# Kernel tuning notes

Hardware: AMD Instinct MI355X
Metric: run time of the kernel (lower is better)

## Reference

```python
import jax, jax.numpy as jnp
import numpy as np

TOP_K = 512  # int(node_num * K) = int(2048 * 0.25)
NEG = -1.0e12
SLOPE = 0.01  # nn.LeakyReLU default negative_slope


def setup_inputs() -> dict:
    key = jax.random.key(0)
    k1, k2, k3, k4 = jax.random.split(key, 4)
    B, N, in_c, out_c, gs = 8, 2048, 128, 128, 128
    x = jax.random.normal(k1, (B, N, in_c), dtype=jnp.float32)
    W = jax.random.normal(k2, (in_c, out_c), dtype=jnp.float32) * (1.0 / np.sqrt(in_c))
    a = jax.random.normal(k3, (2 * out_c, 1), dtype=jnp.float32) * (1.0 / np.sqrt(2 * out_c))
    GL = jax.random.normal(k4, (N, gs), dtype=jnp.float32) * (1.0 / np.sqrt(gs))
    return {"x": x, "W": W, "a": a, "GL": GL}


def reference(x, W, a, GL):
    B, N, _ = x.shape
    out_c = W.shape[1]
    # learned adjacency: softmax(relu(GL GL^T)) + I  -> [N, N]
    adj = jax.nn.softmax(jax.nn.relu(GL @ GL.T), axis=-1) + jnp.eye(N, dtype=GL.dtype)
    h = x @ W  # [B, N, out_c]
    # e[b,i,j] = LeakyReLU( [h_i ; h_j] . a ) = LeakyReLU( h_i.a1 + h_j.a2 )
    # (avoids materializing the [B, N*N, 2*out_c] concat of the original)
    a1, a2 = a[:out_c, 0], a[out_c:, 0]
    e = jax.nn.leaky_relu((h @ a1)[:, :, None] + (h @ a2)[:, None, :], SLOPE)  # [B,N,N]
    att = jnp.where(adj[None] > 0, e, NEG)
    # top-k along dim=1 (rows, per column j): transpose so that axis is last
    att_t = jnp.swapaxes(att, 1, 2)  # [B, Nj, Ni]
    _, idx = jax.lax.top_k(att_t, TOP_K)  # idx: [B, Nj, TOP_K]
    b_ix = jnp.arange(B)[:, None, None]
    j_ix = jnp.arange(N)[None, :, None]
    mask_t = jnp.zeros_like(att_t).at[b_ix, j_ix, idx].set(1.0)
    mask = jnp.swapaxes(mask_t, 1, 2)  # [B, Ni, Nj]
    att = jax.nn.softmax(att * mask, axis=2)
    h_prime = jax.nn.relu(att @ h)  # [B, N, out_c]
    return jnp.swapaxes(h_prime, -2, -1)  # [B, out_c, N]
```

## Files before the change

### kernel.cpp

```cpp
#include <hip/hip_runtime.h>
#include <hip/hip_bf16.h>
#include <math.h>


#define B_ 8
#define N_ 2048
#define C_ 128
#define TOPK_ 512
#define NCH_ 32
#define CL_ 64
#define NP1_ 2050

#define H_OFF    ((size_t)0)
#define P_OFF    (H_OFF + (size_t)B_*N_*C_)
#define Q_OFF    (P_OFF + (size_t)B_*N_)
#define QS_OFF   (Q_OFF + (size_t)B_*N_)
#define US_OFF   (QS_OFF + (size_t)B_*N_)
#define VS_OFF   (US_OFF + (size_t)B_*N_)
#define SRT_OFF  (VS_OFF + (size_t)B_*N_)
#define SUS_OFF  (SRT_OFF + (size_t)B_*N_)
#define PVS_OFF  (SUS_OFF + (size_t)B_*NP1_)
#define SUL_OFF  (PVS_OFF + (size_t)B_*NP1_)
#define PVL_OFF  (SUL_OFF + (size_t)B_*N_*128)
#define TOTU_OFF (PVL_OFF + (size_t)B_*N_*128)
#define TOTV_OFF (TOTU_OFF + (size_t)B_*NCH_*128)
#define MR_OFF   (TOTV_OFF + (size_t)B_*NCH_*128)
#define MPART_OFF (MR_OFF + (size_t)B_*C_)
#define PTHR_OFF (MPART_OFF + (size_t)B_*32*C_)
#define ITHR_OFF (PTHR_OFF + (size_t)B_)

__device__ __forceinline__ unsigned enc_f(float f) {
  unsigned b = __float_as_uint(f);
  return b ^ ((b >> 31) ? 0xFFFFFFFFu : 0x80000000u);
}
__device__ __forceinline__ float dec_f(unsigned e) {
  unsigned b = (e & 0x80000000u) ? (e ^ 0x80000000u) : ~e;
  return __uint_as_float(b);
}
__device__ __forceinline__ unsigned long long sxor64(unsigned long long v, int m) {
  int lo = __shfl_xor((int)(unsigned)(v & 0xffffffffULL), m, 64);
  int hi = __shfl_xor((int)(unsigned)(v >> 32), m, 64);
  return (((unsigned long long)(unsigned)hi) << 32) | (unsigned)lo;
}

__global__ __launch_bounds__(256) void k_gemm(const float* __restrict__ x,
                                              const float* __restrict__ W,
                                              const float* __restrict__ a,
                                              float* __restrict__ h,
                                              float* __restrict__ p,
                                              float* __restrict__ q,
                                              float* __restrict__ mpart) {
  __shared__ float Wl[64 * 128];
  __shared__ float xl[64 * 68];
  __shared__ float a1l[128], a2l[128];
  __shared__ float redp[64][16], redq[64][16];
  const int t = threadIdx.x;
  const int r0 = blockIdx.x * 64;
  if (t < 128) { a1l[t] = a[t]; a2l[t] = a[128 + t]; }
  const int cg = t & 15, rp = t >> 4;
  float acc[4][8];
#pragma unroll
  for (int r = 0; r < 4; ++r)
#pragma unroll
    for (int j = 0; j < 8; ++j) acc[r][j] = 0.f;

  for (int kc = 0; kc < 2; ++kc) {
    __syncthreads();
    const float4* W4 = (const float4*)(W + (size_t)kc * 64 * 128);
    float4* Wl4 = (float4*)Wl;
#pragma unroll
    for (int i = 0; i < 8; ++i) Wl4[t + 256 * i] = W4[t + 256 * i];
#pragma unroll
    for (int i = 0; i < 4; ++i) {
      int idx = t + 256 * i;
      int row = idx >> 4, c4i = idx & 15;
      float4 v = *(const float4*)(x + (size_t)(r0 + row) * 128 + kc * 64 + c4i * 4);
      ((float4*)xl)[row * 17 + c4i] = v;
    }
    __syncthreads();
    for (int k = 0; k < 64; ++k) {
      const float4* Wr = (const float4*)(Wl + k * 128);
      float4 w0 = Wr[cg];
      float4 w1 = Wr[cg + 16];
#pragma unroll
      for (int r = 0; r < 4; ++r) {
        float xv = xl[(4 * rp + r) * 68 + k];
        acc[r][0] = fmaf(xv, w0.x, acc[r][0]);
        acc[r][1] = fmaf(xv, w0.y, acc[r][1]);
        acc[r][2] = fmaf(xv, w0.z, acc[r][2]);
        acc[r][3] = fmaf(xv, w0.w, acc[r][3]);
        acc[r][4] = fmaf(xv, w1.x, acc[r][4]);
        acc[r][5] = fmaf(xv, w1.y, acc[r][5]);
        acc[r][6] = fmaf(xv, w1.z, acc[r][6]);
        acc[r][7] = fmaf(xv, w1.w, acc[r][7]);
      }
    }
  }
  const int c0 = 4 * cg, c1 = 4 * cg + 64;
  size_t hb = (size_t)r0 * 128;
  __syncthreads();
  float* scratch = xl;
#pragma unroll
  for (int r = 0; r < 4; ++r) {
    int row = 4 * rp + r;
    *(float4*)(h + hb + (size_t)row * 128 + c0) =
        make_float4(acc[r][0], acc[r][1], acc[r][2], acc[r][3]);
    *(float4*)(h + hb + (size_t)row * 128 + c1) =
        make_float4(acc[r][4], acc[r][5], acc[r][6], acc[r][7]);
    float pp = 0.f, qq = 0.f;
#pragma unroll
    for (int j = 0; j < 4; ++j) {
      pp = fmaf(acc[r][j], a1l[c0 + j], pp);
      qq = fmaf(acc[r][j], a2l[c0 + j], qq);
      pp = fmaf(acc[r][4 + j], a1l[c1 + j], pp);
      qq = fmaf(acc[r][4 + j], a2l[c1 + j], qq);
    }
    redp[row][cg] = pp; redq[row][cg] = qq;
  }
#pragma unroll
  for (int j = 0; j < 4; ++j) {
    scratch[rp * 128 + c0 + j] = acc[0][j] + acc[1][j] + acc[2][j] + acc[3][j];
    scratch[rp * 128 + c1 + j] = acc[0][4+j] + acc[1][4+j] + acc[2][4+j] + acc[3][4+j];
  }
  __syncthreads();
  if (t < 64) {
    float sp = 0.f, sq = 0.f;
#pragma unroll
    for (int i = 0; i < 16; ++i) { sp += redp[t][i]; sq += redq[t][i]; }
    p[r0 + t] = sp;
    q[r0 + t] = sq;
  }
  if (t < 128) {
    float s = 0.f;
#pragma unroll
    for (int rr = 0; rr < 16; ++rr) s += scratch[rr * 128 + t];
    mpart[(size_t)blockIdx.x * 128 + t] = s;
  }
}

__global__ __launch_bounds__(1024) void k_sort(const float* __restrict__ q,
                                               const float* __restrict__ p,
                                               const float* __restrict__ mpart,
                                               float* __restrict__ q_s,
                                               float* __restrict__ u_s,
                                               float* __restrict__ v_s,
                                               int* __restrict__ srt,
                                               float* __restrict__ SUS,
                                               float* __restrict__ PVS,
                                               float* __restrict__ pthr,
                                               int* __restrict__ ithr,
                                               float* __restrict__ mrw) {
  __shared__ unsigned long long sh[N_];
  __shared__ float2 sa[1024], sb[1024];
  __shared__ float red[8][128];
  const int blk = blockIdx.x, t = threadIdx.x;

  if (blk >= 2 * B_) {
    const int b = blk - 2 * B_;
    const int c = t & 127, i = t >> 7;
    float s = 0.f;
#pragma unroll
    for (int j = 4 * i; j < 4 * i + 4; ++j)
      s += mpart[(size_t)(b * 32 + j) * 128 + c];
    red[i][c] = s;
    __syncthreads();
    if (t < 128) {
      float s2 = 0.f;
#pragma unroll
      for (int i2 = 0; i2 < 8; ++i2) s2 += red[i2][t];
      mrw[b * 128 + t] = fmaxf(s2 * (1.0f / (float)N_), 0.f);
    }
    return;
  }

  const bool isP = blk >= B_;
  const int b = isP ? blk - B_ : blk;
  const float* src = isP ? p : q;
  float2 f2 = *(const float2*)(src + b * N_ + 2 * t);
  unsigned k0 = enc_f(f2.x), k1 = enc_f(f2.y);
  if (isP) { k0 = ~k0; k1 = ~k1; }
  unsigned long long r0 = ((unsigned long long)k0 << 32) | (unsigned)(2 * t);
  unsigned long long r1 = ((unsigned long long)k1 << 32) | (unsigned)(2 * t + 1);

  for (int k = 2; k <= N_; k <<= 1) {
    const bool up = (((2 * t) & k) == 0);
    int j = k >> 1;
    for (; j >= 128; j >>= 1) {
      *(ulonglong2*)(sh + 2 * t) = make_ulonglong2(r0, r1);
      __syncthreads();
      int pe = (2 * t) ^ j;
      ulonglong2 pp = *(const ulonglong2*)(sh + pe);
      bool lower = (((2 * t) & j) == 0);
      bool kmin = (up == lower);
      r0 = kmin ? (r0 < pp.x ? r0 : pp.x) : (r0 > pp.x ? r0 : pp.x);
      r1 = kmin ? (r1 < pp.y ? r1 : pp.y) : (r1 > pp.y ? r1 : pp.y);
      __syncthreads();
    }
    for (; j >= 2; j >>= 1) {
      int j2 = j >> 1;
      unsigned long long p0 = sxor64(r0, j2);
      unsigned long long p1 = sxor64(r1, j2);
      bool lower = ((t & j2) == 0);
      bool kmin = (up == lower);
      r0 = kmin ? (r0 < p0 ? r0 : p0) : (r0 > p0 ? r0 : p0);
      r1 = kmin ? (r1 < p1 ? r1 : p1) : (r1 > p1 ? r1 : p1);
    }
    if (up) {
      if (r0 > r1) { unsigned long long tm = r0; r0 = r1; r1 = tm; }
    } else {
      if (r1 > r0) { unsigned long long tm = r0; r0 = r1; r1 = tm; }
    }
  }

  if (isP) {
    if (t == 255) {
      unsigned key = (unsigned)(r1 >> 32);
      pthr[b] = dec_f(~key);
      ithr[b] = (int)(unsigned)(r1 & 0xffffffffULL);
    }
    return;
  }
  float v0 = dec_f((unsigned)(r0 >> 32));
  float v1 = dec_f((unsigned)(r1 >> 32));
  int i0 = (int)(unsigned)(r0 & 0xffffffffULL);
  int i1 = (int)(unsigned)(r1 & 0xffffffffULL);
  float u0 = __expf(v0), u1 = __expf(v1);
  float w0 = __expf(0.01f * v0), w1 = __expf(0.01f * v1);
  *(float2*)(q_s + b * N_ + 2 * t) = make_float2(v0, v1);
  *(float2*)(u_s + b * N_ + 2 * t) = make_float2(u0, u1);
  *(float2*)(v_s + b * N_ + 2 * t) = make_float2(w0, w1);
  *(int2*)(srt + b * N_ + 2 * t) = make_int2(i0, i1);
  float pu = u0 + u1, pw = w0 + w1;
  sa[1023 - t].x = pu;
  sa[t].y = pw;
  __syncthreads();
  float2* cur = sa; float2* nxt = sb;
  for (int off = 1; off < 1024; off <<= 1) {
    float2 vv = cur[t];
    if (t >= off) { float2 o = cur[t - off]; vv.x += o.x; vv.y += o.y; }
    nxt[t] = vv;
    __syncthreads();
    float2* tmp = cur; cur = nxt; nxt = tmp;
  }
  float PSt = cur[1023 - t].x;
  float PPt = cur[t].y;
  *(float2*)(SUS + (size_t)b * NP1_ + 2 * t) = make_float2(PSt, PSt - u0);
  *(float2*)(PVS + (size_t)b * NP1_ + 2 * t) = make_float2(PPt - pw, PPt - w1);
  if (t == 1023) {
    SUS[(size_t)b * NP1_ + N_] = 0.f;
    PVS[(size_t)b * NP1_ + N_] = PPt;
  }
}

__global__ __launch_bounds__(256) void k_scanA(const float* __restrict__ h,
                                               const float* __restrict__ u_s,
                                               const float* __restrict__ v_s,
                                               const int* __restrict__ srt,
                                               float* __restrict__ SUl,
                                               float* __restrict__ PVl,
                                               float* __restrict__ totU,
                                               float* __restrict__ totV) {
  __shared__ float hl[CL_][128];
  __shared__ float ul[CL_], vl[CL_];
  __shared__ int sl[CL_];
  const int b = blockIdx.x >> 5, ch = blockIdx.x & 31;
  const int t = threadIdx.x;
  const int base = b * N_ + ch * CL_;
  if (t < CL_) { ul[t] = u_s[base + t]; vl[t] = v_s[base + t]; sl[t] = srt[base + t]; }
  __syncthreads();
  {
    const int c4 = t & 31, rr = t >> 5;
#pragma unroll
    for (int i = 0; i < 8; ++i) {
      int tt = rr + 8 * i;
      float4 v = *(const float4*)(h + ((size_t)b * N_ + sl[tt]) * 128 + 4 * c4);
      *(float4*)(&hl[tt][4 * c4]) = v;
    }
  }
  __syncthreads();
  if (t < 128) {
    const int c = t;
    float run = 0.f;
    for (int tt = CL_ - 1; tt >= 0; --tt) {
      run = fmaf(ul[tt], hl[tt][c], run);
      SUl[((size_t)(base + tt)) * 128 + c] = run;
    }
    totU[(size_t)(b * NCH_ + ch) * 128 + c] = run;
  } else {
    const int c = t - 128;
    float run2 = 0.f;
    for (int tt = 0; tt < CL_; ++tt) {
      PVl[((size_t)(base + tt)) * 128 + c] = run2;
      run2 = fmaf(vl[tt], hl[tt][c], run2);
    }
    totV[(size_t)(b * NCH_ + ch) * 128 + c] = run2;
  }
}

__global__ __launch_bounds__(256) void k_out(const float* __restrict__ p,
                                             const float* __restrict__ q_s,
                                             const float* __restrict__ pthr,
                                             const int* __restrict__ ithr,
                                             const float* __restrict__ SUS,
                                             const float* __restrict__ PVS,
                                             const float* __restrict__ SUl,
                                             const float* __restrict__ PVl,
                                             const float* __restrict__ totU,
                                             const float* __restrict__ totV,
                                             const float* __restrict__ mrw,
                                             float* __restrict__ out) {
  __shared__ float qs_l[N_];
  __shared__ float res[64 * 129];
  __shared__ float CSUs[(NCH_ + 1) * 128];
  __shared__ float CPVs[(NCH_ + 1) * 128];
  __shared__ float mr[128];
  __shared__ float A_s[64], B_s[64], invD[64];
  __shared__ int lo_s[64], keep_s[64];
  const int b = blockIdx.x >> 5, tile = blockIdx.x & 31;
  const int t = threadIdx.x;
  const int i0 = tile * 64;
  for (int i = t; i < N_; i += 256) qs_l[i] = q_s[b * N_ + i];
  if (t < 128) {
    mr[t] = mrw[b * 128 + t];
    float s = 0.f;
    CSUs[NCH_ * 128 + t] = 0.f;
    for (int cc = NCH_ - 1; cc >= 0; --cc) {
      s += totU[(size_t)(b * NCH_ + cc) * 128 + t];
      CSUs[cc * 128 + t] = s;
    }
  } else {
    const int c2 = t - 128;
    float s2 = 0.f;
    for (int cc = 0; cc < NCH_; ++cc) {
      CPVs[cc * 128 + c2] = s2;
      s2 += totV[(size_t)(b * NCH_ + cc) * 128 + c2];
    }
    CPVs[NCH_ * 128 + c2] = s2;
  }
  __syncthreads();
  if (t < 64) {
    float pv = p[b * N_ + i0 + t];
    float thrv = pthr[b]; int thri = ithr[b];
    bool keep = (pv > thrv) || (pv == thrv && (i0 + t) <= thri);
    keep_s[t] = keep ? 1 : 0;
    float thr = -pv;
    int lo = 0, hi = N_;
    while (lo < hi) { int mid = (lo + hi) >> 1; if (qs_l[mid] < thr) lo = mid + 1; else hi = mid; }
    lo_s[t] = lo;
    float A = __expf(pv), Bv = __expf(0.01f * pv);
    A_s[t] = A; B_s[t] = Bv;
    float sus = SUS[(size_t)b * NP1_ + lo];
    float pvs = PVS[(size_t)b * NP1_ + lo];
    invD[t] = 1.0f / fmaf(A, sus, Bv * pvs);
  }
  __syncthreads();
  const int half = t >> 7, c = t & 127;
#pragma unroll 4
  for (int ii2 = 0; ii2 < 64; ii2 += 2) {
    int ii = ii2 + half;
    float outv;
    if (keep_s[ii]) {
      int lo = lo_s[ii];
      float A = A_s[ii], Bv = B_s[ii];
      float suc, pvc;
      if (lo < N_) {
        int chn = lo >> 6;
        size_t ro = ((size_t)(b * N_ + lo)) * 128;
        suc = SUl[ro + c] + CSUs[(chn + 1) * 128 + c];
        pvc = PVl[ro + c] + CPVs[chn * 128 + c];
      } else {
        suc = 0.f;
        pvc = CPVs[NCH_ * 128 + c];
      }
      outv = fmaxf(fmaf(A, suc, Bv * pvc) * invD[ii], 0.f);
    } else {
      outv = mr[c];
    }
    res[ii * 129 + c] = outv;
  }
  __syncthreads();
#pragma unroll
  for (int pass = 0; pass < 8; ++pass) {
    int cc = (t >> 4) + pass * 16;
    int ii4 = (t & 15) * 4;
    float4 v;
    v.x = res[(ii4 + 0) * 129 + cc];
    v.y = res[(ii4 + 1) * 129 + cc];
    v.z = res[(ii4 + 2) * 129 + cc];
    v.w = res[(ii4 + 3) * 129 + cc];
    *(float4*)(out + ((size_t)(b * C_ + cc)) * N_ + i0 + ii4) = v;
  }
}

extern "C" void kernel_launch(void* const* d_in, const int* in_sizes, int n_in,
                              void* d_out, int out_size, void* d_ws, size_t ws_size,
                              hipStream_t stream) {
  (void)in_sizes; (void)n_in; (void)out_size; (void)ws_size;
  const float* x = (const float*)d_in[0];
  const float* W = (const float*)d_in[1];
  const float* a = (const float*)d_in[2];
  float* out = (float*)d_out;
  float* ws = (float*)d_ws;

  float* h    = ws + H_OFF;
  float* p    = ws + P_OFF;
  float* q    = ws + Q_OFF;
  float* q_s  = ws + QS_OFF;
  float* u_s  = ws + US_OFF;
  float* v_s  = ws + VS_OFF;
  int*   srt  = (int*)(ws + SRT_OFF);
  float* SUS  = ws + SUS_OFF;
  float* PVS  = ws + PVS_OFF;
  float* SUl  = ws + SUL_OFF;
  float* PVl  = ws + PVL_OFF;
  float* totU = ws + TOTU_OFF;
  float* totV = ws + TOTV_OFF;
  float* mrw  = ws + MR_OFF;
  float* mpart = ws + MPART_OFF;
  float* pthr = ws + PTHR_OFF;
  int*   ithr = (int*)(ws + ITHR_OFF);

  k_gemm<<<dim3((B_ * N_) / 64), dim3(256), 0, stream>>>(x, W, a, h, p, q, mpart);
  k_sort<<<dim3(3 * B_), dim3(1024), 0, stream>>>(q, p, mpart, q_s, u_s, v_s, srt, SUS, PVS, pthr, ithr, mrw);
  k_scanA<<<dim3(B_ * NCH_), dim3(256), 0, stream>>>(h, u_s, v_s, srt, SUl, PVl, totU, totV);
  k_out<<<dim3(B_ * 32), dim3(256), 0, stream>>>(p, q_s, pthr, ithr, SUS, PVS, SUl, PVl, totU, totV, mrw, out);
}
```

Before: 112.5 us.

## Compute p,q via folded W·a and overlap sorting with the h GEMM

Adds a small kernel that folds W·a1 and W·a2 into two vectors and computes p and q directly from x, so the sort no longer has to wait for the full h GEMM. The sort (now 4 elements per thread with 512 threads) and the h GEMM are merged into one launch through a shared-memory union, letting the sort blocks run alongside the GEMM blocks. The mean-reduction kernel stage is removed and its work moves into k_out's prologue. In exchange, x is read twice, the GEMM blocks leave half of their 512 threads idle, and p and q are computed in a different order, which changes their rounding slightly and could flip near-tied top-k selections.

Result: faster. 106.3 us (-5.5%).

```diff
diff --git a/kernel.cpp b/kernel.cpp
--- a/kernel.cpp
+++ b/kernel.cpp
@@ -1,5 +1,4 @@
 #include <hip/hip_runtime.h>
-#include <hip/hip_bf16.h>
 #include <math.h>
 
 
@@ -9,7 +8,8 @@
 #define TOPK_ 512
 #define NCH_ 32
 #define CL_ 64
-#define NP1_ 2050
+#define NP1_ 2052
+#define SORTB_ (2 * B_)
 
 #define H_OFF    ((size_t)0)
 #define P_OFF    (H_OFF + (size_t)B_*N_*C_)
@@ -24,8 +24,7 @@
 #define PVL_OFF  (SUL_OFF + (size_t)B_*N_*128)
 #define TOTU_OFF (PVL_OFF + (size_t)B_*N_*128)
 #define TOTV_OFF (TOTU_OFF + (size_t)B_*NCH_*128)
-#define MR_OFF   (TOTV_OFF + (size_t)B_*NCH_*128)
-#define MPART_OFF (MR_OFF + (size_t)B_*C_)
+#define MPART_OFF (TOTV_OFF + (size_t)B_*NCH_*128)
 #define PTHR_OFF (MPART_OFF + (size_t)B_*32*C_)
 #define ITHR_OFF (PTHR_OFF + (size_t)B_)
 
@@ -42,22 +41,185 @@
   int hi = __shfl_xor((int)(unsigned)(v >> 32), m, 64);
   return (((unsigned long long)(unsigned)hi) << 32) | (unsigned)lo;
 }
-
-__global__ __launch_bounds__(256) void k_gemm(const float* __restrict__ x,
-                                              const float* __restrict__ W,
-                                              const float* __restrict__ a,
-                                              float* __restrict__ h,
-                                              float* __restrict__ p,
-                                              float* __restrict__ q,
-                                              float* __restrict__ mpart) {
-  __shared__ float Wl[64 * 128];
-  __shared__ float xl[64 * 68];
-  __shared__ float a1l[128], a2l[128];
-  __shared__ float redp[64][16], redq[64][16];
+__device__ __forceinline__ void cswap2(unsigned long long& a, unsigned long long& b, bool up) {
+  bool sw = up ? (a > b) : (b > a);
+  if (sw) { unsigned long long tm = a; a = b; b = tm; }
+}
+
+__global__ __launch_bounds__(256) void k_pq(const float* __restrict__ x,
+                                            const float* __restrict__ W,
+                                            const float* __restrict__ a,
+                                            float* __restrict__ p,
+                                            float* __restrict__ q) {
+  __shared__ float al[256];
+  __shared__ float wa1[128], wa2[128];
   const int t = threadIdx.x;
   const int r0 = blockIdx.x * 64;
-  if (t < 128) { a1l[t] = a[t]; a2l[t] = a[128 + t]; }
-  const int cg = t & 15, rp = t >> 4;
+  al[t] = a[t];
+  __syncthreads();
+  if (t < 128) {
+    const float* Wr = W + (size_t)t * 128;
+    float s1 = 0.f, s2 = 0.f;
+#pragma unroll
+    for (int j = 0; j < 128; j += 4) {
+      float4 wv = *(const float4*)(Wr + j);
+      s1 = fmaf(wv.x, al[j + 0], s1);
+      s1 = fmaf(wv.y, al[j + 1], s1);
+      s1 = fmaf(wv.z, al[j + 2], s1);
+      s1 = fmaf(wv.w, al[j + 3], s1);
+      s2 = fmaf(wv.x, al[128 + j + 0], s2);
+      s2 = fmaf(wv.y, al[128 + j + 1], s2);
+      s2 = fmaf(wv.z, al[128 + j + 2], s2);
+      s2 = fmaf(wv.w, al[128 + j + 3], s2);
+    }
+    wa1[t] = s1; wa2[t] = s2;
+  }
+  __syncthreads();
+  const int row = t >> 2, part = t & 3;
+  const float* xr = x + (size_t)(r0 + row) * 128 + part * 32;
+  const float* w1 = wa1 + part * 32;
+  const float* w2 = wa2 + part * 32;
+  float sp = 0.f, sq = 0.f;
+#pragma unroll
+  for (int i = 0; i < 8; ++i) {
+    float4 xv = *(const float4*)(xr + 4 * i);
+    float4 w1v = *(const float4*)(w1 + 4 * i);
+    float4 w2v = *(const float4*)(w2 + 4 * i);
+    sp = fmaf(xv.x, w1v.x, sp); sp = fmaf(xv.y, w1v.y, sp);
+    sp = fmaf(xv.z, w1v.z, sp); sp = fmaf(xv.w, w1v.w, sp);
+    sq = fmaf(xv.x, w2v.x, sq); sq = fmaf(xv.y, w2v.y, sq);
+    sq = fmaf(xv.z, w2v.z, sq); sq = fmaf(xv.w, w2v.w, sq);
+  }
+  sp += __shfl_xor(sp, 1, 64); sp += __shfl_xor(sp, 2, 64);
+  sq += __shfl_xor(sq, 1, 64); sq += __shfl_xor(sq, 2, 64);
+  if (part == 0) { p[r0 + row] = sp; q[r0 + row] = sq; }
+}
+
+__global__ __launch_bounds__(512, 4) void k_fuse(
+    const float* __restrict__ x, const float* __restrict__ W,
+    float* __restrict__ h, float* __restrict__ mpart,
+    const float* __restrict__ q, const float* __restrict__ p,
+    float* __restrict__ q_s, float* __restrict__ u_s, float* __restrict__ v_s,
+    int* __restrict__ srt, float* __restrict__ SUS, float* __restrict__ PVS,
+    float* __restrict__ pthr, int* __restrict__ ithr) {
+  union __align__(16) SMem {
+    struct { float Wl[64 * 128]; float xl[64 * 68]; } g;
+    struct { unsigned long long sh[N_]; float2 sa[512]; float2 sb[512]; } s;
+  };
+  __shared__ SMem sm;
+  const int blk = blockIdx.x, t = threadIdx.x;
+
+  if (blk < SORTB_) {
+    const bool isP = blk >= B_;
+    const int b = isP ? blk - B_ : blk;
+    const float* src = isP ? p : q;
+    float4 f4 = *(const float4*)(src + b * N_ + 4 * t);
+    unsigned k0 = enc_f(f4.x), k1 = enc_f(f4.y), k2 = enc_f(f4.z), k3 = enc_f(f4.w);
+    if (isP) { k0 = ~k0; k1 = ~k1; k2 = ~k2; k3 = ~k3; }
+    unsigned long long r[4];
+    r[0] = ((unsigned long long)k0 << 32) | (unsigned)(4 * t);
+    r[1] = ((unsigned long long)k1 << 32) | (unsigned)(4 * t + 1);
+    r[2] = ((unsigned long long)k2 << 32) | (unsigned)(4 * t + 2);
+    r[3] = ((unsigned long long)k3 << 32) | (unsigned)(4 * t + 3);
+
+    cswap2(r[0], r[1], true);
+    cswap2(r[2], r[3], false);
+    {
+      const bool up4 = (t & 1) == 0;
+      cswap2(r[0], r[2], up4); cswap2(r[1], r[3], up4);
+      cswap2(r[0], r[1], up4); cswap2(r[2], r[3], up4);
+    }
+    for (int k = 8; k <= N_; k <<= 1) {
+      const bool up = ((4 * t) & k) == 0;
+      int j = k >> 1;
+      for (; j >= 256; j >>= 1) {
+        *(ulonglong2*)(sm.s.sh + 4 * t) = make_ulonglong2(r[0], r[1]);
+        *(ulonglong2*)(sm.s.sh + 4 * t + 2) = make_ulonglong2(r[2], r[3]);
+        __syncthreads();
+        int pt = t ^ (j >> 2);
+        ulonglong2 pa = *(const ulonglong2*)(sm.s.sh + 4 * pt);
+        ulonglong2 pb = *(const ulonglong2*)(sm.s.sh + 4 * pt + 2);
+        bool lower = (t & (j >> 2)) == 0;
+        bool kmin = (up == lower);
+        r[0] = kmin ? (r[0] < pa.x ? r[0] : pa.x) : (r[0] > pa.x ? r[0] : pa.x);
+        r[1] = kmin ? (r[1] < pa.y ? r[1] : pa.y) : (r[1] > pa.y ? r[1] : pa.y);
+        r[2] = kmin ? (r[2] < pb.x ? r[2] : pb.x) : (r[2] > pb.x ? r[2] : pb.x);
+        r[3] = kmin ? (r[3] < pb.y ? r[3] : pb.y) : (r[3] > pb.y ? r[3] : pb.y);
+        __syncthreads();
+      }
+      for (; j >= 4; j >>= 1) {
+        int ld = j >> 2;
+        unsigned long long p0 = sxor64(r[0], ld), p1 = sxor64(r[1], ld);
+        unsigned long long p2 = sxor64(r[2], ld), p3 = sxor64(r[3], ld);
+        bool lower = (t & ld) == 0;
+        bool kmin = (up == lower);
+        r[0] = kmin ? (r[0] < p0 ? r[0] : p0) : (r[0] > p0 ? r[0] : p0);
+        r[1] = kmin ? (r[1] < p1 ? r[1] : p1) : (r[1] > p1 ? r[1] : p1);
+        r[2] = kmin ? (r[2] < p2 ? r[2] : p2) : (r[2] > p2 ? r[2] : p2);
+        r[3] = kmin ? (r[3] < p3 ? r[3] : p3) : (r[3] > p3 ? r[3] : p3);
+      }
+      cswap2(r[0], r[2], up); cswap2(r[1], r[3], up);
+      cswap2(r[0], r[1], up); cswap2(r[2], r[3], up);
+    }
+
+    if (isP) {
+      if (t == 127) {
+        unsigned key = (unsigned)(r[3] >> 32);
+        pthr[b] = dec_f(~key);
+        ithr[b] = (int)(unsigned)(r[3] & 0xffffffffULL);
+      }
+      return;
+    }
+    float v[4], u[4], w[4]; int id[4];
+#pragma unroll
+    for (int s = 0; s < 4; ++s) {
+      v[s] = dec_f((unsigned)(r[s] >> 32));
+      id[s] = (int)(unsigned)(r[s] & 0xffffffffULL);
+      u[s] = __expf(v[s]);
+      w[s] = __expf(0.01f * v[s]);
+    }
+    *(float4*)(q_s + b * N_ + 4 * t) = make_float4(v[0], v[1], v[2], v[3]);
+    *(float4*)(u_s + b * N_ + 4 * t) = make_float4(u[0], u[1], u[2], u[3]);
+    *(float4*)(v_s + b * N_ + 4 * t) = make_float4(w[0], w[1], w[2], w[3]);
+    *(int4*)(srt + b * N_ + 4 * t) = make_int4(id[0], id[1], id[2], id[3]);
+    float pu = u[0] + u[1] + u[2] + u[3];
+    float pw = w[0] + w[1] + w[2] + w[3];
+    sm.s.sa[511 - t].x = pu;
+    sm.s.sa[t].y = pw;
+    __syncthreads();
+    float2* cur = sm.s.sa; float2* nxt = sm.s.sb;
+    for (int off = 1; off < 512; off <<= 1) {
+      float2 vv = cur[t];
+      if (t >= off) { float2 o = cur[t - off]; vv.x += o.x; vv.y += o.y; }
+      nxt[t] = vv;
+      __syncthreads();
+      float2* tmp = cur; cur = nxt; nxt = tmp;
+    }
+    float PSt = cur[511 - t].x;
+    float PPt = cur[t].y;
+    float su0 = PSt;
+    float su1 = su0 - u[0];
+    float su2 = su1 - u[1];
+    float su3 = su2 - u[2];
+    *(float4*)(SUS + (size_t)b * NP1_ + 4 * t) = make_float4(su0, su1, su2, su3);
+    float pv3 = PPt - w[3];
+    float pv2 = pv3 - w[2];
+    float pv1 = pv2 - w[1];
+    float pv0 = pv1 - w[0];
+    *(float4*)(PVS + (size_t)b * NP1_ + 4 * t) = make_float4(pv0, pv1, pv2, pv3);
+    if (t == 511) {
+      SUS[(size_t)b * NP1_ + N_] = 0.f;
+      PVS[(size_t)b * NP1_ + N_] = PPt;
+    }
+    return;
+  }
+
+  float* Wl = sm.g.Wl;
+  float* xl = sm.g.xl;
+  const int g = blk - SORTB_;
+  const int r0 = g * 64;
+  const int cg = t & 15, rp = (t >> 4) & 15;
+  const bool act = t < 256;
   float acc[4][8];
 #pragma unroll
   for (int r = 0; r < 4; ++r)
@@ -69,30 +231,32 @@
     const float4* W4 = (const float4*)(W + (size_t)kc * 64 * 128);
     float4* Wl4 = (float4*)Wl;
 #pragma unroll
-    for (int i = 0; i < 8; ++i) Wl4[t + 256 * i] = W4[t + 256 * i];
-#pragma unroll
-    for (int i = 0; i < 4; ++i) {
-      int idx = t + 256 * i;
+    for (int i = 0; i < 4; ++i) Wl4[t + 512 * i] = W4[t + 512 * i];
+#pragma unroll
+    for (int i = 0; i < 2; ++i) {
+      int idx = t + 512 * i;
       int row = idx >> 4, c4i = idx & 15;
       float4 v = *(const float4*)(x + (size_t)(r0 + row) * 128 + kc * 64 + c4i * 4);
       ((float4*)xl)[row * 17 + c4i] = v;
     }
     __syncthreads();
-    for (int k = 0; k < 64; ++k) {
-      const float4* Wr = (const float4*)(Wl + k * 128);
-      float4 w0 = Wr[cg];
-      float4 w1 = Wr[cg + 16];
-#pragma unroll
-      for (int r = 0; r < 4; ++r) {
-        float xv = xl[(4 * rp + r) * 68 + k];
-        acc[r][0] = fmaf(xv, w0.x, acc[r][0]);
-        acc[r][1] = fmaf(xv, w0.y, acc[r][1]);
-        acc[r][2] = fmaf(xv, w0.z, acc[r][2]);
-        acc[r][3] = fmaf(xv, w0.w, acc[r][3]);
-        acc[r][4] = fmaf(xv, w1.x, acc[r][4]);
-        acc[r][5] = fmaf(xv, w1.y, acc[r][5]);
-        acc[r][6] = fmaf(xv, w1.z, acc[r][6]);
-        acc[r][7] = fmaf(xv, w1.w, acc[r][7]);
+    if (act) {
+      for (int k = 0; k < 64; ++k) {
+        const float4* Wr = (const float4*)(Wl + k * 128);
+        float4 w0 = Wr[cg];
+        float4 w1 = Wr[cg + 16];
+#pragma unroll
+        for (int r = 0; r < 4; ++r) {
+          float xv = xl[(4 * rp + r) * 68 + k];
+          acc[r][0] = fmaf(xv, w0.x, acc[r][0]);
+          acc[r][1] = fmaf(xv, w0.y, acc[r][1]);
+          acc[r][2] = fmaf(xv, w0.z, acc[r][2]);
+          acc[r][3] = fmaf(xv, w0.w, acc[r][3]);
+          acc[r][4] = fmaf(xv, w1.x, acc[r][4]);
+          acc[r][5] = fmaf(xv, w1.y, acc[r][5]);
+          acc[r][6] = fmaf(xv, w1.z, acc[r][6]);
+          acc[r][7] = fmaf(xv, w1.w, acc[r][7]);
+        }
       }
     }
   }
@@ -100,155 +264,27 @@
   size_t hb = (size_t)r0 * 128;
   __syncthreads();
   float* scratch = xl;
-#pragma unroll
-  for (int r = 0; r < 4; ++r) {
-    int row = 4 * rp + r;
-    *(float4*)(h + hb + (size_t)row * 128 + c0) =
-        make_float4(acc[r][0], acc[r][1], acc[r][2], acc[r][3]);
-    *(float4*)(h + hb + (size_t)row * 128 + c1) =
-        make_float4(acc[r][4], acc[r][5], acc[r][6], acc[r][7]);
-    float pp = 0.f, qq = 0.f;
+  if (act) {
+#pragma unroll
+    for (int r = 0; r < 4; ++r) {
+      int row = 4 * rp + r;
+      *(float4*)(h + hb + (size_t)row * 128 + c0) =
+          make_float4(acc[r][0], acc[r][1], acc[r][2], acc[r][3]);
+      *(float4*)(h + hb + (size_t)row * 128 + c1) =
+          make_float4(acc[r][4], acc[r][5], acc[r][6], acc[r][7]);
+    }
 #pragma unroll
     for (int j = 0; j < 4; ++j) {
-      pp = fmaf(acc[r][j], a1l[c0 + j], pp);
-      qq = fmaf(acc[r][j], a2l[c0 + j], qq);
-      pp = fmaf(acc[r][4 + j], a1l[c1 + j], pp);
-      qq = fmaf(acc[r][4 + j], a2l[c1 + j], qq);
-    }
-    redp[row][cg] = pp; redq[row][cg] = qq;
-  }
-#pragma unroll
-  for (int j = 0; j < 4; ++j) {
-    scratch[rp * 128 + c0 + j] = acc[0][j] + acc[1][j] + acc[2][j] + acc[3][j];
-    scratch[rp * 128 + c1 + j] = acc[0][4+j] + acc[1][4+j] + acc[2][4+j] + acc[3][4+j];
-  }
-  __syncthreads();
-  if (t < 64) {
-    float sp = 0.f, sq = 0.f;
-#pragma unroll
-    for (int i = 0; i < 16; ++i) { sp += redp[t][i]; sq += redq[t][i]; }
-    p[r0 + t] = sp;
-    q[r0 + t] = sq;
-  }
+      scratch[rp * 128 + c0 + j] = acc[0][j] + acc[1][j] + acc[2][j] + acc[3][j];
+      scratch[rp * 128 + c1 + j] = acc[0][4 + j] + acc[1][4 + j] + acc[2][4 + j] + acc[3][4 + j];
+    }
+  }
+  __syncthreads();
   if (t < 128) {
     float s = 0.f;
 #pragma unroll
     for (int rr = 0; rr < 16; ++rr) s += scratch[rr * 128 + t];
-    mpart[(size_t)blockIdx.x * 128 + t] = s;
-  }
-}
-
-__global__ __launch_bounds__(1024) void k_sort(const float* __restrict__ q,
-                                               const float* __restrict__ p,
-                                               const float* __restrict__ mpart,
-                                               float* __restrict__ q_s,
-                                               float* __restrict__ u_s,
-                                               float* __restrict__ v_s,
-                                               int* __restrict__ srt,
-                                               float* __restrict__ SUS,
-                                               float* __restrict__ PVS,
-                                               float* __restrict__ pthr,
-                                               int* __restrict__ ithr,
-                                               float* __restrict__ mrw) {
-  __shared__ unsigned long long sh[N_];
-  __shared__ float2 sa[1024], sb[1024];
-  __shared__ float red[8][128];
-  const int blk = blockIdx.x, t = threadIdx.x;
-
-  if (blk >= 2 * B_) {
-    const int b = blk - 2 * B_;
-    const int c = t & 127, i = t >> 7;
-    float s = 0.f;
-#pragma unroll
-    for (int j = 4 * i; j < 4 * i + 4; ++j)
-      s += mpart[(size_t)(b * 32 + j) * 128 + c];
-    red[i][c] = s;
-    __syncthreads();
-    if (t < 128) {
-      float s2 = 0.f;
-#pragma unroll
-      for (int i2 = 0; i2 < 8; ++i2) s2 += red[i2][t];
-      mrw[b * 128 + t] = fmaxf(s2 * (1.0f / (float)N_), 0.f);
-    }
-    return;
-  }
-
-  const bool isP = blk >= B_;
-  const int b = isP ? blk - B_ : blk;
-  const float* src = isP ? p : q;
-  float2 f2 = *(const float2*)(src + b * N_ + 2 * t);
-  unsigned k0 = enc_f(f2.x), k1 = enc_f(f2.y);
-  if (isP) { k0 = ~k0; k1 = ~k1; }
-  unsigned long long r0 = ((unsigned long long)k0 << 32) | (unsigned)(2 * t);
-  unsigned long long r1 = ((unsigned long long)k1 << 32) | (unsigned)(2 * t + 1);
-
-  for (int k = 2; k <= N_; k <<= 1) {
-    const bool up = (((2 * t) & k) == 0);
-    int j = k >> 1;
-    for (; j >= 128; j >>= 1) {
-      *(ulonglong2*)(sh + 2 * t) = make_ulonglong2(r0, r1);
-      __syncthreads();
-      int pe = (2 * t) ^ j;
-      ulonglong2 pp = *(const ulonglong2*)(sh + pe);
-      bool lower = (((2 * t) & j) == 0);
-      bool kmin = (up == lower);
-      r0 = kmin ? (r0 < pp.x ? r0 : pp.x) : (r0 > pp.x ? r0 : pp.x);
-      r1 = kmin ? (r1 < pp.y ? r1 : pp.y) : (r1 > pp.y ? r1 : pp.y);
-      __syncthreads();
-    }
-    for (; j >= 2; j >>= 1) {
-      int j2 = j >> 1;
-      unsigned long long p0 = sxor64(r0, j2);
-      unsigned long long p1 = sxor64(r1, j2);
-      bool lower = ((t & j2) == 0);
-      bool kmin = (up == lower);
-      r0 = kmin ? (r0 < p0 ? r0 : p0) : (r0 > p0 ? r0 : p0);
-      r1 = kmin ? (r1 < p1 ? r1 : p1) : (r1 > p1 ? r1 : p1);
-    }
-    if (up) {
-      if (r0 > r1) { unsigned long long tm = r0; r0 = r1; r1 = tm; }
-    } else {
-      if (r1 > r0) { unsigned long long tm = r0; r0 = r1; r1 = tm; }
-    }
-  }
-
-  if (isP) {
-    if (t == 255) {
-      unsigned key = (unsigned)(r1 >> 32);
-      pthr[b] = dec_f(~key);
-      ithr[b] = (int)(unsigned)(r1 & 0xffffffffULL);
-    }
-    return;
-  }
-  float v0 = dec_f((unsigned)(r0 >> 32));
-  float v1 = dec_f((unsigned)(r1 >> 32));
-  int i0 = (int)(unsigned)(r0 & 0xffffffffULL);
-  int i1 = (int)(unsigned)(r1 & 0xffffffffULL);
-  float u0 = __expf(v0), u1 = __expf(v1);
-  float w0 = __expf(0.01f * v0), w1 = __expf(0.01f * v1);
-  *(float2*)(q_s + b * N_ + 2 * t) = make_float2(v0, v1);
-  *(float2*)(u_s + b * N_ + 2 * t) = make_float2(u0, u1);
-  *(float2*)(v_s + b * N_ + 2 * t) = make_float2(w0, w1);
-  *(int2*)(srt + b * N_ + 2 * t) = make_int2(i0, i1);
-  float pu = u0 + u1, pw = w0 + w1;
-  sa[1023 - t].x = pu;
-  sa[t].y = pw;
-  __syncthreads();
-  float2* cur = sa; float2* nxt = sb;
-  for (int off = 1; off < 1024; off <<= 1) {
-    float2 vv = cur[t];
-    if (t >= off) { float2 o = cur[t - off]; vv.x += o.x; vv.y += o.y; }
-    nxt[t] = vv;
-    __syncthreads();
-    float2* tmp = cur; cur = nxt; nxt = tmp;
-  }
-  float PSt = cur[1023 - t].x;
-  float PPt = cur[t].y;
-  *(float2*)(SUS + (size_t)b * NP1_ + 2 * t) = make_float2(PSt, PSt - u0);
-  *(float2*)(PVS + (size_t)b * NP1_ + 2 * t) = make_float2(PPt - pw, PPt - w1);
-  if (t == 1023) {
-    SUS[(size_t)b * NP1_ + N_] = 0.f;
-    PVS[(size_t)b * NP1_ + N_] = PPt;
+    mpart[(size_t)g * 128 + t] = s;
   }
 }
 
@@ -307,7 +343,7 @@
                                              const float* __restrict__ PVl,
                                              const float* __restrict__ totU,
                                              const float* __restrict__ totV,
-                                             const float* __restrict__ mrw,
+                                             const float* __restrict__ mpart,
                                              float* __restrict__ out) {
   __shared__ float qs_l[N_];
   __shared__ float res[64 * 129];
@@ -321,7 +357,10 @@
   const int i0 = tile * 64;
   for (int i = t; i < N_; i += 256) qs_l[i] = q_s[b * N_ + i];
   if (t < 128) {
-    mr[t] = mrw[b * 128 + t];
+    float ms = 0.f;
+#pragma unroll
+    for (int j = 0; j < 32; ++j) ms += mpart[(size_t)(b * 32 + j) * 128 + t];
+    mr[t] = fmaxf(ms * (1.0f / (float)N_), 0.f);
     float s = 0.f;
     CSUs[NCH_ * 128 + t] = 0.f;
     for (int cc = NCH_ - 1; cc >= 0; --cc) {
@@ -415,13 +454,13 @@
   float* PVl  = ws + PVL_OFF;
   float* totU = ws + TOTU_OFF;
   float* totV = ws + TOTV_OFF;
-  float* mrw  = ws + MR_OFF;
   float* mpart = ws + MPART_OFF;
   float* pthr = ws + PTHR_OFF;
   int*   ithr = (int*)(ws + ITHR_OFF);
 
-  k_gemm<<<dim3((B_ * N_) / 64), dim3(256), 0, stream>>>(x, W, a, h, p, q, mpart);
-  k_sort<<<dim3(3 * B_), dim3(1024), 0, stream>>>(q, p, mpart, q_s, u_s, v_s, srt, SUS, PVS, pthr, ithr, mrw);
+  k_pq<<<dim3((B_ * N_) / 64), dim3(256), 0, stream>>>(x, W, a, p, q);
+  k_fuse<<<dim3(SORTB_ + (B_ * N_) / 64), dim3(512), 0, stream>>>(
+      x, W, h, mpart, q, p, q_s, u_s, v_s, srt, SUS, PVS, pthr, ithr);
   k_scanA<<<dim3(B_ * NCH_), dim3(256), 0, stream>>>(h, u_s, v_s, srt, SUl, PVl, totU, totV);
-  k_out<<<dim3(B_ * 32), dim3(256), 0, stream>>>(p, q_s, pthr, ithr, SUS, PVS, SUl, PVl, totU, totV, mrw, out);
-}
+  k_out<<<dim3(B_ * 32), dim3(256), 0, stream>>>(p, q_s, pthr, ithr, SUS, PVS, SUl, PVl, totU, totV, mpart, out);
+}
```

## Fuse GEMM and sort kernels, computing p/q via folded W·a projection

Applied to the files above, without the earlier changes.

Merges the GEMM and sort kernels into one launch. The sort blocks compute p and q directly from x using a precomputed W·a vector instead of waiting on h, so the sort runs concurrently with the GEMM blocks. The mean-reduction block is dropped and the per-column mean is folded into k_out by summing mpart there. The GEMM blocks now launch 1024 threads with only 256 doing math, which wastes threads and may lower occupancy. Computing p and q via (W·a) also changes floating-point summation order, which could flip near-tie sort orders.

Result: slower. 138.4 us (+23.1%).

```diff
diff --git a/kernel.cpp b/kernel.cpp
--- a/kernel.cpp
+++ b/kernel.cpp
@@ -1,5 +1,4 @@
 #include <hip/hip_runtime.h>
-#include <hip/hip_bf16.h>
 #include <math.h>
 
 
@@ -9,7 +8,8 @@
 #define TOPK_ 512
 #define NCH_ 32
 #define CL_ 64
-#define NP1_ 2050
+#define NP1_ 2052
+#define SORTB_ (2 * B_)
 
 #define H_OFF    ((size_t)0)
 #define P_OFF    (H_OFF + (size_t)B_*N_*C_)
@@ -24,8 +24,7 @@
 #define PVL_OFF  (SUL_OFF + (size_t)B_*N_*128)
 #define TOTU_OFF (PVL_OFF + (size_t)B_*N_*128)
 #define TOTV_OFF (TOTU_OFF + (size_t)B_*NCH_*128)
-#define MR_OFF   (TOTV_OFF + (size_t)B_*NCH_*128)
-#define MPART_OFF (MR_OFF + (size_t)B_*C_)
+#define MPART_OFF (TOTV_OFF + (size_t)B_*NCH_*128)
 #define PTHR_OFF (MPART_OFF + (size_t)B_*32*C_)
 #define ITHR_OFF (PTHR_OFF + (size_t)B_)
 
@@ -43,21 +42,142 @@
   return (((unsigned long long)(unsigned)hi) << 32) | (unsigned)lo;
 }
 
-__global__ __launch_bounds__(256) void k_gemm(const float* __restrict__ x,
-                                              const float* __restrict__ W,
-                                              const float* __restrict__ a,
-                                              float* __restrict__ h,
-                                              float* __restrict__ p,
-                                              float* __restrict__ q,
-                                              float* __restrict__ mpart) {
-  __shared__ float Wl[64 * 128];
-  __shared__ float xl[64 * 68];
-  __shared__ float a1l[128], a2l[128];
-  __shared__ float redp[64][16], redq[64][16];
-  const int t = threadIdx.x;
-  const int r0 = blockIdx.x * 64;
-  if (t < 128) { a1l[t] = a[t]; a2l[t] = a[128 + t]; }
-  const int cg = t & 15, rp = t >> 4;
+__global__ __launch_bounds__(1024, 4) void k_fuse(
+    const float* __restrict__ x, const float* __restrict__ W,
+    const float* __restrict__ a,
+    float* __restrict__ h, float* __restrict__ mpart,
+    float* __restrict__ p,
+    float* __restrict__ q_s, float* __restrict__ u_s, float* __restrict__ v_s,
+    int* __restrict__ srt, float* __restrict__ SUS, float* __restrict__ PVS,
+    float* __restrict__ pthr, int* __restrict__ ithr) {
+  union __align__(16) SMem {
+    struct { float Wl[64 * 128]; float xl[64 * 68]; } g;
+    struct {
+      unsigned long long sh[N_];
+      float2 sa[1024], sb[1024];
+      float al[128], wav[128];
+    } s;
+  };
+  __shared__ SMem sm;
+  const int blk = blockIdx.x, t = threadIdx.x;
+
+  if (blk < SORTB_) {
+    const bool isP = blk >= B_;
+    const int b = isP ? blk - B_ : blk;
+    if (t < 128) sm.s.al[t] = a[(isP ? 0 : 128) + t];
+    __syncthreads();
+    if (t < 128) {
+      const float* Wr = W + (size_t)t * 128;
+      float s1 = 0.f;
+#pragma unroll
+      for (int j = 0; j < 128; j += 4) {
+        float4 wv = *(const float4*)(Wr + j);
+        s1 = fmaf(wv.x, sm.s.al[j + 0], s1);
+        s1 = fmaf(wv.y, sm.s.al[j + 1], s1);
+        s1 = fmaf(wv.z, sm.s.al[j + 2], s1);
+        s1 = fmaf(wv.w, sm.s.al[j + 3], s1);
+      }
+      sm.s.wav[t] = s1;
+    }
+    __syncthreads();
+    float gv0 = 0.f, gv1 = 0.f;
+    {
+      const float* x0 = x + ((size_t)b * N_ + 2 * t) * 128;
+#pragma unroll
+      for (int j = 0; j < 128; j += 4) {
+        float4 w4 = *(const float4*)(sm.s.wav + j);
+        float4 xa = *(const float4*)(x0 + j);
+        float4 xb = *(const float4*)(x0 + 128 + j);
+        gv0 = fmaf(xa.x, w4.x, gv0); gv0 = fmaf(xa.y, w4.y, gv0);
+        gv0 = fmaf(xa.z, w4.z, gv0); gv0 = fmaf(xa.w, w4.w, gv0);
+        gv1 = fmaf(xb.x, w4.x, gv1); gv1 = fmaf(xb.y, w4.y, gv1);
+        gv1 = fmaf(xb.z, w4.z, gv1); gv1 = fmaf(xb.w, w4.w, gv1);
+      }
+    }
+    if (isP) *(float2*)(p + b * N_ + 2 * t) = make_float2(gv0, gv1);
+
+    unsigned k0 = enc_f(gv0), k1 = enc_f(gv1);
+    if (isP) { k0 = ~k0; k1 = ~k1; }
+    unsigned long long r0 = ((unsigned long long)k0 << 32) | (unsigned)(2 * t);
+    unsigned long long r1 = ((unsigned long long)k1 << 32) | (unsigned)(2 * t + 1);
+
+    for (int k = 2; k <= N_; k <<= 1) {
+      const bool up = (((2 * t) & k) == 0);
+      int j = k >> 1;
+      for (; j >= 128; j >>= 1) {
+        *(ulonglong2*)(sm.s.sh + 2 * t) = make_ulonglong2(r0, r1);
+        __syncthreads();
+        int pe = (2 * t) ^ j;
+        ulonglong2 pp = *(const ulonglong2*)(sm.s.sh + pe);
+        bool lower = (((2 * t) & j) == 0);
+        bool kmin = (up == lower);
+        r0 = kmin ? (r0 < pp.x ? r0 : pp.x) : (r0 > pp.x ? r0 : pp.x);
+        r1 = kmin ? (r1 < pp.y ? r1 : pp.y) : (r1 > pp.y ? r1 : pp.y);
+        __syncthreads();
+      }
+      for (; j >= 2; j >>= 1) {
+        int j2 = j >> 1;
+        unsigned long long p0 = sxor64(r0, j2);
+        unsigned long long p1 = sxor64(r1, j2);
+        bool lower = ((t & j2) == 0);
+        bool kmin = (up == lower);
+        r0 = kmin ? (r0 < p0 ? r0 : p0) : (r0 > p0 ? r0 : p0);
+        r1 = kmin ? (r1 < p1 ? r1 : p1) : (r1 > p1 ? r1 : p1);
+      }
+      if (up) {
+        if (r0 > r1) { unsigned long long tm = r0; r0 = r1; r1 = tm; }
+      } else {
+        if (r1 > r0) { unsigned long long tm = r0; r0 = r1; r1 = tm; }
+      }
+    }
+
+    if (isP) {
+      if (t == 255) {
+        unsigned key = (unsigned)(r1 >> 32);
+        pthr[b] = dec_f(~key);
+        ithr[b] = (int)(unsigned)(r1 & 0xffffffffULL);
+      }
+      return;
+    }
+    float qv0 = dec_f((unsigned)(r0 >> 32));
+    float qv1 = dec_f((unsigned)(r1 >> 32));
+    int i0 = (int)(unsigned)(r0 & 0xffffffffULL);
+    int i1 = (int)(unsigned)(r1 & 0xffffffffULL);
+    float u0 = __expf(qv0), u1 = __expf(qv1);
+    float w0 = __expf(0.01f * qv0), w1 = __expf(0.01f * qv1);
+    *(float2*)(q_s + b * N_ + 2 * t) = make_float2(qv0, qv1);
+    *(float2*)(u_s + b * N_ + 2 * t) = make_float2(u0, u1);
+    *(float2*)(v_s + b * N_ + 2 * t) = make_float2(w0, w1);
+    *(int2*)(srt + b * N_ + 2 * t) = make_int2(i0, i1);
+    float pu = u0 + u1, pw = w0 + w1;
+    sm.s.sa[1023 - t].x = pu;
+    sm.s.sa[t].y = pw;
+    __syncthreads();
+    float2* cur = sm.s.sa; float2* nxt = sm.s.sb;
+    for (int off = 1; off < 1024; off <<= 1) {
+      float2 vv = cur[t];
+      if (t >= off) { float2 o = cur[t - off]; vv.x += o.x; vv.y += o.y; }
+      nxt[t] = vv;
+      __syncthreads();
+      float2* tmp = cur; cur = nxt; nxt = tmp;
+    }
+    float PSt = cur[1023 - t].x;
+    float PPt = cur[t].y;
+    *(float2*)(SUS + (size_t)b * NP1_ + 2 * t) = make_float2(PSt, PSt - u0);
+    *(float2*)(PVS + (size_t)b * NP1_ + 2 * t) = make_float2(PPt - pw, PPt - w1);
+    if (t == 1023) {
+      SUS[(size_t)b * NP1_ + N_] = 0.f;
+      PVS[(size_t)b * NP1_ + N_] = PPt;
+    }
+    return;
+  }
+
+  float* Wl = sm.g.Wl;
+  float* xl = sm.g.xl;
+  const int g = blk - SORTB_;
+  const int r0 = g * 64;
+  const int cg = t & 15, rp = (t >> 4) & 15;
+  const bool act = t < 256;
   float acc[4][8];
 #pragma unroll
   for (int r = 0; r < 4; ++r)
@@ -69,30 +189,30 @@
     const float4* W4 = (const float4*)(W + (size_t)kc * 64 * 128);
     float4* Wl4 = (float4*)Wl;
 #pragma unroll
-    for (int i = 0; i < 8; ++i) Wl4[t + 256 * i] = W4[t + 256 * i];
-#pragma unroll
-    for (int i = 0; i < 4; ++i) {
-      int idx = t + 256 * i;
-      int row = idx >> 4, c4i = idx & 15;
+    for (int i = 0; i < 2; ++i) Wl4[t + 1024 * i] = W4[t + 1024 * i];
+    {
+      int row = t >> 4, c4i = t & 15;
       float4 v = *(const float4*)(x + (size_t)(r0 + row) * 128 + kc * 64 + c4i * 4);
       ((float4*)xl)[row * 17 + c4i] = v;
     }
     __syncthreads();
-    for (int k = 0; k < 64; ++k) {
-      const float4* Wr = (const float4*)(Wl + k * 128);
-      float4 w0 = Wr[cg];
-      float4 w1 = Wr[cg + 16];
-#pragma unroll
-      for (int r = 0; r < 4; ++r) {
-        float xv = xl[(4 * rp + r) * 68 + k];
-        acc[r][0] = fmaf(xv, w0.x, acc[r][0]);
-        acc[r][1] = fmaf(xv, w0.y, acc[r][1]);
-        acc[r][2] = fmaf(xv, w0.z, acc[r][2]);
-        acc[r][3] = fmaf(xv, w0.w, acc[r][3]);
-        acc[r][4] = fmaf(xv, w1.x, acc[r][4]);
-        acc[r][5] = fmaf(xv, w1.y, acc[r][5]);
-        acc[r][6] = fmaf(xv, w1.z, acc[r][6]);
-        acc[r][7] = fmaf(xv, w1.w, acc[r][7]);
+    if (act) {
+      for (int k = 0; k < 64; ++k) {
+        const float4* Wr = (const float4*)(Wl + k * 128);
+        float4 w0 = Wr[cg];
+        float4 w1 = Wr[cg + 16];
+#pragma unroll
+        for (int r = 0; r < 4; ++r) {
+          float xv = xl[(4 * rp + r) * 68 + k];
+          acc[r][0] = fmaf(xv, w0.x, acc[r][0]);
+          acc[r][1] = fmaf(xv, w0.y, acc[r][1]);
+          acc[r][2] = fmaf(xv, w0.z, acc[r][2]);
+          acc[r][3] = fmaf(xv, w0.w, acc[r][3]);
+          acc[r][4] = fmaf(xv, w1.x, acc[r][4]);
+          acc[r][5] = fmaf(xv, w1.y, acc[r][5]);
+          acc[r][6] = fmaf(xv, w1.z, acc[r][6]);
+          acc[r][7] = fmaf(xv, w1.w, acc[r][7]);
+        }
       }
     }
   }
@@ -100,155 +220,27 @@
   size_t hb = (size_t)r0 * 128;
   __syncthreads();
   float* scratch = xl;
-#pragma unroll
-  for (int r = 0; r < 4; ++r) {
-    int row = 4 * rp + r;
-    *(float4*)(h + hb + (size_t)row * 128 + c0) =
-        make_float4(acc[r][0], acc[r][1], acc[r][2], acc[r][3]);
-    *(float4*)(h + hb + (size_t)row * 128 + c1) =
-        make_float4(acc[r][4], acc[r][5], acc[r][6], acc[r][7]);
-    float pp = 0.f, qq = 0.f;
+  if (act) {
+#pragma unroll
+    for (int r = 0; r < 4; ++r) {
+      int row = 4 * rp + r;
+      *(float4*)(h + hb + (size_t)row * 128 + c0) =
+          make_float4(acc[r][0], acc[r][1], acc[r][2], acc[r][3]);
+      *(float4*)(h + hb + (size_t)row * 128 + c1) =
+          make_float4(acc[r][4], acc[r][5], acc[r][6], acc[r][7]);
+    }
 #pragma unroll
     for (int j = 0; j < 4; ++j) {
-      pp = fmaf(acc[r][j], a1l[c0 + j], pp);
-      qq = fmaf(acc[r][j], a2l[c0 + j], qq);
-      pp = fmaf(acc[r][4 + j], a1l[c1 + j], pp);
-      qq = fmaf(acc[r][4 + j], a2l[c1 + j], qq);
-    }
-    redp[row][cg] = pp; redq[row][cg] = qq;
-  }
-#pragma unroll
-  for (int j = 0; j < 4; ++j) {
-    scratch[rp * 128 + c0 + j] = acc[0][j] + acc[1][j] + acc[2][j] + acc[3][j];
-    scratch[rp * 128 + c1 + j] = acc[0][4+j] + acc[1][4+j] + acc[2][4+j] + acc[3][4+j];
-  }
-  __syncthreads();
-  if (t < 64) {
-    float sp = 0.f, sq = 0.f;
-#pragma unroll
-    for (int i = 0; i < 16; ++i) { sp += redp[t][i]; sq += redq[t][i]; }
-    p[r0 + t] = sp;
-    q[r0 + t] = sq;
-  }
+      scratch[rp * 128 + c0 + j] = acc[0][j] + acc[1][j] + acc[2][j] + acc[3][j];
+      scratch[rp * 128 + c1 + j] = acc[0][4 + j] + acc[1][4 + j] + acc[2][4 + j] + acc[3][4 + j];
+    }
+  }
+  __syncthreads();
   if (t < 128) {
     float s = 0.f;
 #pragma unroll
     for (int rr = 0; rr < 16; ++rr) s += scratch[rr * 128 + t];
-    mpart[(size_t)blockIdx.x * 128 + t] = s;
-  }
-}
-
-__global__ __launch_bounds__(1024) void k_sort(const float* __restrict__ q,
-                                               const float* __restrict__ p,
-                                               const float* __restrict__ mpart,
-                                               float* __restrict__ q_s,
-                                               float* __restrict__ u_s,
-                                               float* __restrict__ v_s,
-                                               int* __restrict__ srt,
-                                               float* __restrict__ SUS,
-                                               float* __restrict__ PVS,
-                                               float* __restrict__ pthr,
-                                               int* __restrict__ ithr,
-                                               float* __restrict__ mrw) {
-  __shared__ unsigned long long sh[N_];
-  __shared__ float2 sa[1024], sb[1024];
-  __shared__ float red[8][128];
-  const int blk = blockIdx.x, t = threadIdx.x;
-
-  if (blk >= 2 * B_) {
-    const int b = blk - 2 * B_;
-    const int c = t & 127, i = t >> 7;
-    float s = 0.f;
-#pragma unroll
-    for (int j = 4 * i; j < 4 * i + 4; ++j)
-      s += mpart[(size_t)(b * 32 + j) * 128 + c];
-    red[i][c] = s;
-    __syncthreads();
-    if (t < 128) {
-      float s2 = 0.f;
-#pragma unroll
-      for (int i2 = 0; i2 < 8; ++i2) s2 += red[i2][t];
-      mrw[b * 128 + t] = fmaxf(s2 * (1.0f / (float)N_), 0.f);
-    }
-    return;
-  }
-
-  const bool isP = blk >= B_;
-  const int b = isP ? blk - B_ : blk;
-  const float* src = isP ? p : q;
-  float2 f2 = *(const float2*)(src + b * N_ + 2 * t);
-  unsigned k0 = enc_f(f2.x), k1 = enc_f(f2.y);
-  if (isP) { k0 = ~k0; k1 = ~k1; }
-  unsigned long long r0 = ((unsigned long long)k0 << 32) | (unsigned)(2 * t);
-  unsigned long long r1 = ((unsigned long long)k1 << 32) | (unsigned)(2 * t + 1);
-
-  for (int k = 2; k <= N_; k <<= 1) {
-    const bool up = (((2 * t) & k) == 0);
-    int j = k >> 1;
-    for (; j >= 128; j >>= 1) {
-      *(ulonglong2*)(sh + 2 * t) = make_ulonglong2(r0, r1);
-      __syncthreads();
-      int pe = (2 * t) ^ j;
-      ulonglong2 pp = *(const ulonglong2*)(sh + pe);
-      bool lower = (((2 * t) & j) == 0);
-      bool kmin = (up == lower);
-      r0 = kmin ? (r0 < pp.x ? r0 : pp.x) : (r0 > pp.x ? r0 : pp.x);
-      r1 = kmin ? (r1 < pp.y ? r1 : pp.y) : (r1 > pp.y ? r1 : pp.y);
-      __syncthreads();
-    }
-    for (; j >= 2; j >>= 1) {
-      int j2 = j >> 1;
-      unsigned long long p0 = sxor64(r0, j2);
-      unsigned long long p1 = sxor64(r1, j2);
-      bool lower = ((t & j2) == 0);
-      bool kmin = (up == lower);
-      r0 = kmin ? (r0 < p0 ? r0 : p0) : (r0 > p0 ? r0 : p0);
-      r1 = kmin ? (r1 < p1 ? r1 : p1) : (r1 > p1 ? r1 : p1);
-    }
-    if (up) {
-      if (r0 > r1) { unsigned long long tm = r0; r0 = r1; r1 = tm; }
-    } else {
-      if (r1 > r0) { unsigned long long tm = r0; r0 = r1; r1 = tm; }
-    }
-  }
-
-  if (isP) {
-    if (t == 255) {
-      unsigned key = (unsigned)(r1 >> 32);
-      pthr[b] = dec_f(~key);
-      ithr[b] = (int)(unsigned)(r1 & 0xffffffffULL);
-    }
-    return;
-  }
-  float v0 = dec_f((unsigned)(r0 >> 32));
-  float v1 = dec_f((unsigned)(r1 >> 32));
-  int i0 = (int)(unsigned)(r0 & 0xffffffffULL);
-  int i1 = (int)(unsigned)(r1 & 0xffffffffULL);
-  float u0 = __expf(v0), u1 = __expf(v1);
-  float w0 = __expf(0.01f * v0), w1 = __expf(0.01f * v1);
-  *(float2*)(q_s + b * N_ + 2 * t) = make_float2(v0, v1);
-  *(float2*)(u_s + b * N_ + 2 * t) = make_float2(u0, u1);
-  *(float2*)(v_s + b * N_ + 2 * t) = make_float2(w0, w1);
-  *(int2*)(srt + b * N_ + 2 * t) = make_int2(i0, i1);
-  float pu = u0 + u1, pw = w0 + w1;
-  sa[1023 - t].x = pu;
-  sa[t].y = pw;
-  __syncthreads();
-  float2* cur = sa; float2* nxt = sb;
-  for (int off = 1; off < 1024; off <<= 1) {
-    float2 vv = cur[t];
-    if (t >= off) { float2 o = cur[t - off]; vv.x += o.x; vv.y += o.y; }
-    nxt[t] = vv;
-    __syncthreads();
-    float2* tmp = cur; cur = nxt; nxt = tmp;
-  }
-  float PSt = cur[1023 - t].x;
-  float PPt = cur[t].y;
-  *(float2*)(SUS + (size_t)b * NP1_ + 2 * t) = make_float2(PSt, PSt - u0);
-  *(float2*)(PVS + (size_t)b * NP1_ + 2 * t) = make_float2(PPt - pw, PPt - w1);
-  if (t == 1023) {
-    SUS[(size_t)b * NP1_ + N_] = 0.f;
-    PVS[(size_t)b * NP1_ + N_] = PPt;
+    mpart[(size_t)g * 128 + t] = s;
   }
 }
 
@@ -307,7 +299,7 @@
                                              const float* __restrict__ PVl,
                                              const float* __restrict__ totU,
                                              const float* __restrict__ totV,
-                                             const float* __restrict__ mrw,
+                                             const float* __restrict__ mpart,
                                              float* __restrict__ out) {
   __shared__ float qs_l[N_];
   __shared__ float res[64 * 129];
@@ -321,7 +313,10 @@
   const int i0 = tile * 64;
   for (int i = t; i < N_; i += 256) qs_l[i] = q_s[b * N_ + i];
   if (t < 128) {
-    mr[t] = mrw[b * 128 + t];
+    float ms = 0.f;
+#pragma unroll
+    for (int j = 0; j < 32; ++j) ms += mpart[(size_t)(b * 32 + j) * 128 + t];
+    mr[t] = fmaxf(ms * (1.0f / (float)N_), 0.f);
     float s = 0.f;
     CSUs[NCH_ * 128 + t] = 0.f;
     for (int cc = NCH_ - 1; cc >= 0; --cc) {
@@ -404,7 +399,6 @@
 
   float* h    = ws + H_OFF;
   float* p    = ws + P_OFF;
-  float* q    = ws + Q_OFF;
   float* q_s  = ws + QS_OFF;
   float* u_s  = ws + US_OFF;
   float* v_s  = ws + VS_OFF;
@@ -415,13 +409,12 @@
   float* PVl  = ws + PVL_OFF;
   float* totU = ws + TOTU_OFF;
   float* totV = ws + TOTV_OFF;
-  float* mrw  = ws + MR_OFF;
   float* mpart = ws + MPART_OFF;
   float* pthr = ws + PTHR_OFF;
   int*   ithr = (int*)(ws + ITHR_OFF);
 
-  k_gemm<<<dim3((B_ * N_) / 64), dim3(256), 0, stream>>>(x, W, a, h, p, q, mpart);
-  k_sort<<<dim3(3 * B_), dim3(1024), 0, stream>>>(q, p, mpart, q_s, u_s, v_s, srt, SUS, PVS, pthr, ithr, mrw);
+  k_fuse<<<dim3(SORTB_ + (B_ * N_) / 64), dim3(1024), 0, stream>>>(
+      x, W, a, h, mpart, p, q_s, u_s, v_s, srt, SUS, PVS, pthr, ithr);
   k_scanA<<<dim3(B_ * NCH_), dim3(256), 0, stream>>>(h, u_s, v_s, srt, SUl, PVl, totU, totV);
-  k_out<<<dim3(B_ * 32), dim3(256), 0, stream>>>(p, q_s, pthr, ithr, SUS, PVS, SUl, PVl, totU, totV, mrw, out);
-}
+  k_out<<<dim3(B_ * 32), dim3(256), 0, stream>>>(p, q_s, pthr, ithr, SUS, PVS, SUl, PVl, totU, totV, mpart, out);
+}
```
